# Optimization experiments

Measured on AMD Instinct MI355X. Metric: run time of the kernel, lower is better.

Reference implementation:

```python
import jax, jax.numpy as jnp
import numpy as np

N_NODES = 50000
N_EDGES = 800000
D_IN, D1, D2, D_OUT = 128, 150, 100, 64


def setup_inputs() -> dict:
    key = jax.random.key(0)
    ks = jax.random.split(key, 10)
    x = jax.random.normal(ks[0], (N_NODES, D_IN), dtype=jnp.float32)
    src = jax.random.randint(ks[1], (N_EDGES,), 0, N_NODES, dtype=jnp.int32)
    dst = jax.random.randint(ks[2], (N_EDGES,), 0, N_NODES, dtype=jnp.int32)
    s1 = 1.0 / np.sqrt(D_IN)
    s2 = 1.0 / np.sqrt(D1)
    s3 = 1.0 / np.sqrt(D2)
    W1 = jax.random.uniform(ks[3], (D_IN, D1), jnp.float32, -s1, s1)
    b1 = jnp.zeros((D1,), jnp.float32)
    Wn = jax.random.uniform(ks[4], (D1, D2), jnp.float32, -s2, s2)
    Ws = jax.random.uniform(ks[5], (D1, D2), jnp.float32, -s2, s2)
    b2 = jnp.zeros((D2,), jnp.float32)
    W3 = jax.random.uniform(ks[6], (D2, D_OUT), jnp.float32, -s3, s3)
    b3 = jnp.zeros((D_OUT,), jnp.float32)
    return {"x": x, "src": src, "dst": dst, "W1": W1, "b1": b1,
            "Wn": Wn, "Ws": Ws, "b2": b2, "W3": W3, "b3": b3}


def _degrees(src, dst, n):
    ones = jnp.ones(src.shape[0], jnp.float32)
    deg_out = jax.ops.segment_sum(ones, src, num_segments=n)
    deg_in = jax.ops.segment_sum(ones, dst, num_segments=n)
    return deg_out, deg_in


def reference(x, src, dst, W1, b1, Wn, Ws, b2, W3, b3):
    n = x.shape[0]
    deg_out, deg_in = _degrees(src, dst, n)
    norm_out = jax.lax.rsqrt(jnp.maximum(deg_out, 1.0))  # [N]
    norm_in = jax.lax.rsqrt(jnp.maximum(deg_in, 1.0))    # [N]

    # --- GraphConv (norm='both'): D_in^{-1/2} A D_out^{-1/2} X W + b ---
    h = x * norm_out[:, None]                                   # [N, D_IN]
    agg = jax.ops.segment_sum(h[src], dst, num_segments=n)      # [N, D_IN]
    h = (agg * norm_in[:, None]) @ W1 + b1                      # [N, D1]
    h = jax.nn.elu(h)

    # --- SAGEConv (mean): fc_self(h) + fc_neigh(mean_neighbors(h)) + b ---
    neigh_sum = jax.ops.segment_sum(h[src], dst, num_segments=n)  # [N, D1]
    neigh = neigh_sum / jnp.maximum(deg_in, 1.0)[:, None]
    h = h @ Ws + neigh @ Wn + b2                                  # [N, D2]
    h = jax.nn.elu(h)

    # --- Dense + ELU ---
    out = jax.nn.elu(h @ W3 + b3)                                 # [N, D_OUT]
    return out
```

## Files before the change

### kernel.cpp

```cpp
#include <hip/hip_runtime.h>
#include <math.h>

#define N_NODES 50000
#define N_EDGES 800000
#define D_IN 128
#define D1 150
#define LD1 152
#define D2 100
#define LDP 100
#define D_OUT 64
#define SLOT 64
#define HBLK 64
#define HBIN 12500

#define LDS_K 40

using short8 = __attribute__((ext_vector_type(8))) short;
using f32x4  = __attribute__((ext_vector_type(4))) float;

__device__ __forceinline__ float elu(float v) { return v > 0.0f ? v : expm1f(v); }

__device__ __forceinline__ void split_bf16(float a, unsigned short& h, unsigned short& l) {
    unsigned int bits = __float_as_uint(a);
    unsigned int hb = (bits + 0x8000u) >> 16;
    h = (unsigned short)hb;
    float r = a - __uint_as_float(hb << 16);
    l = (unsigned short)((__float_as_uint(r) + 0x8000u) >> 16);
}

__device__ __forceinline__ void split8(const float4 a, const float4 b, short8& h, short8& l) {
    float f[8] = {a.x, a.y, a.z, a.w, b.x, b.y, b.z, b.w};
#pragma unroll
    for (int i = 0; i < 8; ++i) {
        unsigned short hh, ll;
        split_bf16(f[i], hh, ll);
        h[i] = (short)hh; l[i] = (short)ll;
    }
}

__device__ __forceinline__ float4 g_load4(const float* p) { return *(const float4*)p; }

__device__ __forceinline__ float4 g_load4_guard(const float* row, int kbase, int Klim, bool rowok) {
    float4 v;
    v.x = (rowok && kbase + 0 < Klim) ? row[kbase + 0] : 0.0f;
    v.y = (rowok && kbase + 1 < Klim) ? row[kbase + 1] : 0.0f;
    v.z = (rowok && kbase + 2 < Klim) ? row[kbase + 2] : 0.0f;
    v.w = (rowok && kbase + 3 < Klim) ? row[kbase + 3] : 0.0f;
    return v;
}

__device__ __forceinline__ void barrier_lgkm() {
    asm volatile("s_waitcnt lgkmcnt(0)\n\ts_barrier" ::: "memory");
    __builtin_amdgcn_sched_barrier(0);
}

__global__ __launch_bounds__(256) void hist_kernel(const int* __restrict__ src,
                                                   unsigned int* __restrict__ partial) {
    __shared__ unsigned int bins[HBIN];
    int tid = threadIdx.x, b = blockIdx.x;
    for (int i = tid; i < HBIN; i += 256) bins[i] = 0u;
    __syncthreads();
    int e0 = b * (N_EDGES / HBLK);
    int e1 = e0 + (N_EDGES / HBLK);
    for (int e = e0 + tid; e < e1; e += 256) {
        int s = src[e];
        atomicAdd(&bins[s >> 2], 1u << ((s & 3) * 8));
    }
    __syncthreads();
    unsigned int* outp = partial + (size_t)b * HBIN;
    for (int i = tid; i < HBIN; i += 256) outp[i] = bins[i];
}

__global__ __launch_bounds__(256) void norm_kernel(const unsigned int* __restrict__ partial,
                                                   float* __restrict__ norm_out) {
    int i = blockIdx.x * blockDim.x + threadIdx.x;
    if (i >= HBIN) return;
    unsigned int acc = 0;
#pragma unroll
    for (int h = 0; h < HBLK; ++h) acc += partial[(size_t)h * HBIN + i];
#pragma unroll
    for (int j = 0; j < 4; ++j) {
        unsigned int dg = (acc >> (j * 8)) & 0xFF;
        norm_out[i * 4 + j] = rsqrtf(fmaxf((float)dg, 1.0f));
    }
}

__global__ void fill_kernel(const int* __restrict__ src, const int* __restrict__ dst,
                            int* __restrict__ cursor, unsigned short* __restrict__ slots) {
    int e = blockIdx.x * blockDim.x + threadIdx.x;
    if (e < N_EDGES) {
        int d = dst[e], s = src[e];
        int pos = atomicAdd(&cursor[d], 1);
        if (pos < SLOT) slots[d * SLOT + pos] = (unsigned short)s;
    }
}

__global__ __launch_bounds__(256) void gather_x(const float* __restrict__ x,
                                                const float* __restrict__ norm_out,
                                                const int* __restrict__ deg_in,
                                                const unsigned short* __restrict__ slots,
                                                float* __restrict__ agg) {
    int wave = threadIdx.x >> 6;
    int lane = threadIdx.x & 63;
    int half = lane >> 5;
    int c = lane & 31;
    int n = blockIdx.x * 4 + wave;
    if (n >= N_NODES) return;
    int beg = n * SLOT;
    int dg = deg_in[n]; if (dg > SLOT) dg = SLOT;
    int end = beg + dg;
    float4 acc = {0.0f, 0.0f, 0.0f, 0.0f};
    int e = beg + half;
    for (; e + 6 < end; e += 8) {
        int s0 = slots[e];
        int s1 = slots[e + 2];
        int s2 = slots[e + 4];
        int s3 = slots[e + 6];
        float w0 = norm_out[s0], w1 = norm_out[s1];
        float w2 = norm_out[s2], w3 = norm_out[s3];
        float4 v0 = ((const float4*)(x + (size_t)s0 * D_IN))[c];
        float4 v1 = ((const float4*)(x + (size_t)s1 * D_IN))[c];
        float4 v2 = ((const float4*)(x + (size_t)s2 * D_IN))[c];
        float4 v3 = ((const float4*)(x + (size_t)s3 * D_IN))[c];
        acc.x += v0.x * w0 + v1.x * w1 + v2.x * w2 + v3.x * w3;
        acc.y += v0.y * w0 + v1.y * w1 + v2.y * w2 + v3.y * w3;
        acc.z += v0.z * w0 + v1.z * w1 + v2.z * w2 + v3.z * w3;
        acc.w += v0.w * w0 + v1.w * w1 + v2.w * w2 + v3.w * w3;
    }
    for (; e < end; e += 2) {
        int s = slots[e];
        float w = norm_out[s];
        float4 v = ((const float4*)(x + (size_t)s * D_IN))[c];
        acc.x += v.x * w; acc.y += v.y * w; acc.z += v.z * w; acc.w += v.w * w;
    }
    acc.x += __shfl_xor(acc.x, 32);
    acc.y += __shfl_xor(acc.y, 32);
    acc.z += __shfl_xor(acc.z, 32);
    acc.w += __shfl_xor(acc.w, 32);
    if (half == 0) ((float4*)(agg + (size_t)n * D_IN))[c] = acc;
}

__global__ __launch_bounds__(256) void gather_p(const float* __restrict__ p,
                                                const int* __restrict__ deg_in,
                                                const unsigned short* __restrict__ slots,
                                                float* __restrict__ ns) {
    int wave = threadIdx.x >> 6;
    int lane = threadIdx.x & 63;
    int half = lane >> 5;
    int c = lane & 31;
    bool cv = c < D2 / 4;
    int n = blockIdx.x * 4 + wave;
    if (n >= N_NODES) return;
    int beg = n * SLOT;
    int dg = deg_in[n]; if (dg > SLOT) dg = SLOT;
    int end = beg + dg;
    float4 acc = {0.0f, 0.0f, 0.0f, 0.0f};
    if (cv) {
        int e = beg + half;
        for (; e + 6 < end; e += 8) {
            int s0 = slots[e];
            int s1 = slots[e + 2];
            int s2 = slots[e + 4];
            int s3 = slots[e + 6];
            float4 v0 = ((const float4*)(p + (size_t)s0 * LDP))[c];
            float4 v1 = ((const float4*)(p + (size_t)s1 * LDP))[c];
            float4 v2 = ((const float4*)(p + (size_t)s2 * LDP))[c];
            float4 v3 = ((const float4*)(p + (size_t)s3 * LDP))[c];
            acc.x += (v0.x + v1.x) + (v2.x + v3.x);
            acc.y += (v0.y + v1.y) + (v2.y + v3.y);
            acc.z += (v0.z + v1.z) + (v2.z + v3.z);
            acc.w += (v0.w + v1.w) + (v2.w + v3.w);
        }
        for (; e < end; e += 2) {
            int s = slots[e];
            float4 v = ((const float4*)(p + (size_t)s * LDP))[c];
            acc.x += v.x; acc.y += v.y; acc.z += v.z; acc.w += v.w;
        }
    }
    acc.x += __shfl_xor(acc.x, 32);
    acc.y += __shfl_xor(acc.y, 32);
    acc.z += __shfl_xor(acc.z, 32);
    acc.w += __shfl_xor(acc.w, 32);
    if (half == 0 && cv) ((float4*)(ns + (size_t)n * LDP))[c] = acc;
}


template <int K, int KP, int NW, int LDA, int PRE, int EPI, int LDC, int GROUP>
__global__ __launch_bounds__(256, 4)
void gemm_mfma(const float* __restrict__ A, const float* __restrict__ W,
               const float* __restrict__ nsrc, const int* __restrict__ deg,
               const float* __restrict__ bstage, const float* __restrict__ bepi,
               float* __restrict__ C) {
    constexpr int NSTEP = KP / 32;
    constexpr int MBLK = (N_NODES + 63) / 64;
    __shared__ __align__(16) unsigned short AsH[64][LDS_K];
    __shared__ __align__(16) unsigned short AsL[64][LDS_K];
    __shared__ __align__(16) unsigned short BsH[64][LDS_K];
    __shared__ __align__(16) unsigned short BsL[64][LDS_K];

    const int b = blockIdx.x;
    const int cxcd = b & 7;
    const int sIdx = b >> 3;
    const int jj = sIdx / GROUP;
    const int yy = sIdx - jj * GROUP;
    const int xb = cxcd + 8 * jj;
    if (xb >= MBLK) return;
    const int m0 = xb * 64;
    const int n0 = yy * 64;

    const int tid = threadIdx.x;
    const int arow = tid >> 2;
    const int ak = (tid & 3) * 8;
    const int grow = m0 + arow;
    const bool rowok = grow < N_NODES;
    const int bn = tid & 63;
    const int bkg = tid >> 6;
    const int bcol = n0 + bn;
    const int wid = tid >> 6;
    const int lane = tid & 63;
    const int wm = (wid >> 1) * 32;
    const int wn = (wid & 1) * 32;
    const int fr = lane & 15;
    const int fg = lane >> 4;

    float invd = 1.0f;
    if (PRE) {
        int dv = rowok ? deg[grow] : 1;
        invd = 1.0f / fmaxf((float)dv, 1.0f);
    }

    f32x4 acc[2][2];
#pragma unroll
    for (int i = 0; i < 2; ++i)
#pragma unroll
        for (int j = 0; j < 2; ++j) acc[i][j] = {0.0f, 0.0f, 0.0f, 0.0f};

    const float* arp = A + (size_t)grow * LDA;
    const float* nrp = PRE ? (nsrc + (size_t)grow * LDP) : nullptr;

    float4 pa[2][2], pn[2][2];
    float pb[2][8];

    {
        if (rowok && 32 <= K) {
            pa[0][0] = g_load4(arp + ak);
            pa[0][1] = g_load4(arp + ak + 4);
        } else {
            pa[0][0] = g_load4_guard(arp, ak, K, rowok);
            pa[0][1] = g_load4_guard(arp, ak + 4, K, rowok);
        }
        if (PRE) {
            if (rowok && 32 <= K) {
                pn[0][0] = g_load4(nrp + ak);
                pn[0][1] = g_load4(nrp + ak + 4);
            } else {
                pn[0][0] = g_load4_guard(nrp, ak, K, rowok);
                pn[0][1] = g_load4_guard(nrp, ak + 4, K, rowok);
            }
        }
#pragma unroll
        for (int kk = 0; kk < 8; ++kk) {
            int k = bkg * 8 + kk;
            pb[0][kk] = (k < K && bcol < NW) ? W[(size_t)k * NW + bcol] : 0.0f;
        }
    }

#pragma unroll
    for (int t = 0; t < NSTEP; ++t) {
        const int cur = t & 1, nxt = cur ^ 1;
        if (t + 1 < NSTEP) {
            const int k0n = (t + 1) * 32;
            if (rowok && k0n + 32 <= K) {
                pa[nxt][0] = g_load4(arp + k0n + ak);
                pa[nxt][1] = g_load4(arp + k0n + ak + 4);
            } else {
                pa[nxt][0] = g_load4_guard(arp, k0n + ak, K, rowok);
                pa[nxt][1] = g_load4_guard(arp, k0n + ak + 4, K, rowok);
            }
            if (PRE) {
                if (rowok && k0n + 32 <= K) {
                    pn[nxt][0] = g_load4(nrp + k0n + ak);
                    pn[nxt][1] = g_load4(nrp + k0n + ak + 4);
                } else {
                    pn[nxt][0] = g_load4_guard(nrp, k0n + ak, K, rowok);
                    pn[nxt][1] = g_load4_guard(nrp, k0n + ak + 4, K, rowok);
                }
            }
#pragma unroll
            for (int kk = 0; kk < 8; ++kk) {
                int k = k0n + bkg * 8 + kk;
                pb[nxt][kk] = (k < K && bcol < NW) ? W[(size_t)k * NW + bcol] : 0.0f;
            }
        }
        barrier_lgkm();
        {
            const int k0 = t * 32;
            float4 va0 = pa[cur][0], va1 = pa[cur][1];
            if (PRE) {
                const float4 vn0 = pn[cur][0], vn1 = pn[cur][1];
                if (k0 + 32 <= K) {
                    va0.x = elu(va0.x + bstage[k0 + ak + 0] + vn0.x * invd);
                    va0.y = elu(va0.y + bstage[k0 + ak + 1] + vn0.y * invd);
                    va0.z = elu(va0.z + bstage[k0 + ak + 2] + vn0.z * invd);
                    va0.w = elu(va0.w + bstage[k0 + ak + 3] + vn0.w * invd);
                    va1.x = elu(va1.x + bstage[k0 + ak + 4] + vn1.x * invd);
                    va1.y = elu(va1.y + bstage[k0 + ak + 5] + vn1.y * invd);
                    va1.z = elu(va1.z + bstage[k0 + ak + 6] + vn1.z * invd);
                    va1.w = elu(va1.w + bstage[k0 + ak + 7] + vn1.w * invd);
                } else {
                    va0.x = (k0 + ak + 0 < K) ? elu(va0.x + bstage[k0 + ak + 0] + vn0.x * invd) : 0.0f;
                    va0.y = (k0 + ak + 1 < K) ? elu(va0.y + bstage[k0 + ak + 1] + vn0.y * invd) : 0.0f;
                    va0.z = (k0 + ak + 2 < K) ? elu(va0.z + bstage[k0 + ak + 2] + vn0.z * invd) : 0.0f;
                    va0.w = (k0 + ak + 3 < K) ? elu(va0.w + bstage[k0 + ak + 3] + vn0.w * invd) : 0.0f;
                    va1.x = (k0 + ak + 4 < K) ? elu(va1.x + bstage[k0 + ak + 4] + vn1.x * invd) : 0.0f;
                    va1.y = (k0 + ak + 5 < K) ? elu(va1.y + bstage[k0 + ak + 5] + vn1.y * invd) : 0.0f;
                    va1.z = (k0 + ak + 6 < K) ? elu(va1.z + bstage[k0 + ak + 6] + vn1.z * invd) : 0.0f;
                    va1.w = (k0 + ak + 7 < K) ? elu(va1.w + bstage[k0 + ak + 7] + vn1.w * invd) : 0.0f;
                }
            }
            short8 h8, l8;
            split8(va0, va1, h8, l8);
            *(short8*)&AsH[arow][ak] = h8;
            *(short8*)&AsL[arow][ak] = l8;
            float4 vb0, vb1;
            vb0.x = pb[cur][0]; vb0.y = pb[cur][1]; vb0.z = pb[cur][2]; vb0.w = pb[cur][3];
            vb1.x = pb[cur][4]; vb1.y = pb[cur][5]; vb1.z = pb[cur][6]; vb1.w = pb[cur][7];
            split8(vb0, vb1, h8, l8);
            *(short8*)&BsH[bn][bkg * 8] = h8;
            *(short8*)&BsL[bn][bkg * 8] = l8;
        }
        barrier_lgkm();
        {
            short8 ah0 = *(const short8*)&AsH[wm + fr][fg * 8];
            short8 ah1 = *(const short8*)&AsH[wm + 16 + fr][fg * 8];
            short8 al0 = *(const short8*)&AsL[wm + fr][fg * 8];
            short8 al1 = *(const short8*)&AsL[wm + 16 + fr][fg * 8];
            short8 bh0 = *(const short8*)&BsH[wn + fr][fg * 8];
            short8 bh1 = *(const short8*)&BsH[wn + 16 + fr][fg * 8];
            short8 bl0 = *(const short8*)&BsL[wn + fr][fg * 8];
            short8 bl1 = *(const short8*)&BsL[wn + 16 + fr][fg * 8];
            acc[0][0] = __builtin_amdgcn_mfma_f32_16x16x32_bf16(ah0, bh0, acc[0][0], 0, 0, 0);
            acc[0][0] = __builtin_amdgcn_mfma_f32_16x16x32_bf16(al0, bh0, acc[0][0], 0, 0, 0);
            acc[0][0] = __builtin_amdgcn_mfma_f32_16x16x32_bf16(ah0, bl0, acc[0][0], 0, 0, 0);
            acc[0][1] = __builtin_amdgcn_mfma_f32_16x16x32_bf16(ah0, bh1, acc[0][1], 0, 0, 0);
            acc[0][1] = __builtin_amdgcn_mfma_f32_16x16x32_bf16(al0, bh1, acc[0][1], 0, 0, 0);
            acc[0][1] = __builtin_amdgcn_mfma_f32_16x16x32_bf16(ah0, bl1, acc[0][1], 0, 0, 0);
            acc[1][0] = __builtin_amdgcn_mfma_f32_16x16x32_bf16(ah1, bh0, acc[1][0], 0, 0, 0);
            acc[1][0] = __builtin_amdgcn_mfma_f32_16x16x32_bf16(al1, bh0, acc[1][0], 0, 0, 0);
            acc[1][0] = __builtin_amdgcn_mfma_f32_16x16x32_bf16(ah1, bl0, acc[1][0], 0, 0, 0);
            acc[1][1] = __builtin_amdgcn_mfma_f32_16x16x32_bf16(ah1, bh1, acc[1][1], 0, 0, 0);
            acc[1][1] = __builtin_amdgcn_mfma_f32_16x16x32_bf16(al1, bh1, acc[1][1], 0, 0, 0);
            acc[1][1] = __builtin_amdgcn_mfma_f32_16x16x32_bf16(ah1, bl1, acc[1][1], 0, 0, 0);
        }
    }

#pragma unroll
    for (int fi = 0; fi < 2; ++fi) {
#pragma unroll
        for (int r = 0; r < 4; ++r) {
            int row = m0 + wm + fi * 16 + fg * 4 + r;
            if (row >= N_NODES) continue;
            float rmul = 1.0f;
            if (EPI == 1) rmul = rsqrtf(fmaxf((float)deg[row], 1.0f));
#pragma unroll
            for (int fj = 0; fj < 2; ++fj) {
                int col = n0 + wn + fj * 16 + fr;
                if (col >= LDC) continue;
                float v = 0.0f;
                if (col < NW) {
                    v = acc[fi][fj][r];
                    if (EPI == 1) v = elu(v * rmul + bepi[col]);
                    else if (EPI == 3) v = elu(v + bepi[col]);
                }
                C[(size_t)row * LDC + col] = v;
            }
        }
    }
}

__global__ __launch_bounds__(256, 4)
void gemm_dual_mfma(const float* __restrict__ h1, const float* __restrict__ Wn,
                    const float* __restrict__ Ws, float* __restrict__ p,
                    float* __restrict__ h2pre) {
    constexpr int NSTEP = 5;
    constexpr int MBLK = (N_NODES + 63) / 64;
    __shared__ __align__(16) unsigned short AsH[64][LDS_K];
    __shared__ __align__(16) unsigned short AsL[64][LDS_K];
    __shared__ __align__(16) unsigned short BsH[64][LDS_K];
    __shared__ __align__(16) unsigned short BsL[64][LDS_K];

    const int b = blockIdx.x;
    const int cxcd = b & 7;
    const int sIdx = b >> 3;
    const int jj = sIdx >> 2;
    const int yy = sIdx & 3;
    const int xb = cxcd + 8 * jj;
    if (xb >= MBLK) return;
    const int m0 = xb * 64;
    const int n0 = (yy & 1) * 64;
    const float* W = (yy < 2) ? Wn : Ws;

    const int tid = threadIdx.x;
    const int arow = tid >> 2;
    const int ak = (tid & 3) * 8;
    const int grow = m0 + arow;
    const bool rowok = grow < N_NODES;
    const int bn = tid & 63;
    const int bkg = tid >> 6;
    const int bcol = n0 + bn;
    const int wid = tid >> 6;
    const int lane = tid & 63;
    const int wm = (wid >> 1) * 32;
    const int wn = (wid & 1) * 32;
    const int fr = lane & 15;
    const int fg = lane >> 4;

    f32x4 acc[2][2];
#pragma unroll
    for (int i = 0; i < 2; ++i)
#pragma unroll
        for (int j = 0; j < 2; ++j) acc[i][j] = {0.0f, 0.0f, 0.0f, 0.0f};

    const float* arp = h1 + (size_t)grow * LD1;

    float4 pa[2][2];
    float pb[2][8];

    {
        if (rowok) {
            pa[0][0] = g_load4(arp + ak);
            pa[0][1] = g_load4(arp + ak + 4);
        } else {
            pa[0][0] = g_load4_guard(arp, ak, D1, rowok);
            pa[0][1] = g_load4_guard(arp, ak + 4, D1, rowok);
        }
#pragma unroll
        for (int kk = 0; kk < 8; ++kk) {
            int k = bkg * 8 + kk;
            pb[0][kk] = (k < D1 && bcol < D2) ? W[(size_t)k * D2 + bcol] : 0.0f;
        }
    }

#pragma unroll
    for (int t = 0; t < NSTEP; ++t) {
        const int cur = t & 1, nxt = cur ^ 1;
        if (t + 1 < NSTEP) {
            const int k0n = (t + 1) * 32;
            if (rowok && k0n + 32 <= D1) {
                pa[nxt][0] = g_load4(arp + k0n + ak);
                pa[nxt][1] = g_load4(arp + k0n + ak + 4);
            } else {
                pa[nxt][0] = g_load4_guard(arp, k0n + ak, D1, rowok);
                pa[nxt][1] = g_load4_guard(arp, k0n + ak + 4, D1, rowok);
            }
#pragma unroll
            for (int kk = 0; kk < 8; ++kk) {
                int k = k0n + bkg * 8 + kk;
                pb[nxt][kk] = (k < D1 && bcol < D2) ? W[(size_t)k * D2 + bcol] : 0.0f;
            }
        }
        barrier_lgkm();
        {
            short8 h8, l8;
            split8(pa[cur][0], pa[cur][1], h8, l8);
            *(short8*)&AsH[arow][ak] = h8;
            *(short8*)&AsL[arow][ak] = l8;
            float4 vb0, vb1;
            vb0.x = pb[cur][0]; vb0.y = pb[cur][1]; vb0.z = pb[cur][2]; vb0.w = pb[cur][3];
            vb1.x = pb[cur][4]; vb1.y = pb[cur][5]; vb1.z = pb[cur][6]; vb1.w = pb[cur][7];
            split8(vb0, vb1, h8, l8);
            *(short8*)&BsH[bn][bkg * 8] = h8;
            *(short8*)&BsL[bn][bkg * 8] = l8;
        }
        barrier_lgkm();
        {
            short8 ah0 = *(const short8*)&AsH[wm + fr][fg * 8];
            short8 ah1 = *(const short8*)&AsH[wm + 16 + fr][fg * 8];
            short8 al0 = *(const short8*)&AsL[wm + fr][fg * 8];
            short8 al1 = *(const short8*)&AsL[wm + 16 + fr][fg * 8];
            short8 bh0 = *(const short8*)&BsH[wn + fr][fg * 8];
            short8 bh1 = *(const short8*)&BsH[wn + 16 + fr][fg * 8];
            short8 bl0 = *(const short8*)&BsL[wn + fr][fg * 8];
            short8 bl1 = *(const short8*)&BsL[wn + 16 + fr][fg * 8];
            acc[0][0] = __builtin_amdgcn_mfma_f32_16x16x32_bf16(ah0, bh0, acc[0][0], 0, 0, 0);
            acc[0][0] = __builtin_amdgcn_mfma_f32_16x16x32_bf16(al0, bh0, acc[0][0], 0, 0, 0);
            acc[0][0] = __builtin_amdgcn_mfma_f32_16x16x32_bf16(ah0, bl0, acc[0][0], 0, 0, 0);
            acc[0][1] = __builtin_amdgcn_mfma_f32_16x16x32_bf16(ah0, bh1, acc[0][1], 0, 0, 0);
            acc[0][1] = __builtin_amdgcn_mfma_f32_16x16x32_bf16(al0, bh1, acc[0][1], 0, 0, 0);
            acc[0][1] = __builtin_amdgcn_mfma_f32_16x16x32_bf16(ah0, bl1, acc[0][1], 0, 0, 0);
            acc[1][0] = __builtin_amdgcn_mfma_f32_16x16x32_bf16(ah1, bh0, acc[1][0], 0, 0, 0);
            acc[1][0] = __builtin_amdgcn_mfma_f32_16x16x32_bf16(al1, bh0, acc[1][0], 0, 0, 0);
            acc[1][0] = __builtin_amdgcn_mfma_f32_16x16x32_bf16(ah1, bl0, acc[1][0], 0, 0, 0);
            acc[1][1] = __builtin_amdgcn_mfma_f32_16x16x32_bf16(ah1, bh1, acc[1][1], 0, 0, 0);
            acc[1][1] = __builtin_amdgcn_mfma_f32_16x16x32_bf16(al1, bh1, acc[1][1], 0, 0, 0);
            acc[1][1] = __builtin_amdgcn_mfma_f32_16x16x32_bf16(ah1, bl1, acc[1][1], 0, 0, 0);
        }
    }

#pragma unroll
    for (int fi = 0; fi < 2; ++fi) {
#pragma unroll
        for (int r = 0; r < 4; ++r) {
            int row = m0 + wm + fi * 16 + fg * 4 + r;
            if (row >= N_NODES) continue;
#pragma unroll
            for (int fj = 0; fj < 2; ++fj) {
                int col = n0 + wn + fj * 16 + fr;
                float v = acc[fi][fj][r];
                if (col < D2) {
                    if (yy < 2) p[(size_t)row * LDP + col] = v;
                    else        h2pre[(size_t)row * D2 + col] = v;
                }
            }
        }
    }
}

extern "C" void kernel_launch(void* const* d_in, const int* in_sizes, int n_in,
                              void* d_out, int out_size, void* d_ws, size_t ws_size,
                              hipStream_t stream) {
    const float* x  = (const float*)d_in[0];
    const int* src  = (const int*)d_in[1];
    const int* dst  = (const int*)d_in[2];
    const float* W1 = (const float*)d_in[3];
    const float* b1 = (const float*)d_in[4];
    const float* Wn = (const float*)d_in[5];
    const float* Ws = (const float*)d_in[6];
    const float* b2 = (const float*)d_in[7];
    const float* W3 = (const float*)d_in[8];
    const float* b3 = (const float*)d_in[9];
    float* out = (float*)d_out;

    char* wsb = (char*)d_ws;
    unsigned int* partial = (unsigned int*)wsb;
    int*   cursor     = (int*)wsb + 800000;
    float* norm_out   = (float*)wsb + 850000;
    unsigned short* slots = (unsigned short*)((float*)wsb + 900000);
    float* agg        = (float*)wsb + 2500000;
    float* h1         = (float*)wsb + 8900000;
    float* h2pre      = (float*)wsb + 16500000;
    float* p          = agg;
    float* ns         = h1;
    int*   deg_in     = cursor;

    hipMemsetAsync(cursor, 0, N_NODES * sizeof(int), stream);

    hist_kernel<<<HBLK, 256, 0, stream>>>(src, partial);
    fill_kernel<<<(N_EDGES + 255) / 256, 256, 0, stream>>>(src, dst, cursor, slots);
    norm_kernel<<<(HBIN + 255) / 256, 256, 0, stream>>>(partial, norm_out);
    gather_x<<<(N_NODES + 3) / 4, 256, 0, stream>>>(x, norm_out, deg_in, slots, agg);

    const int MB = (N_NODES + 63) / 64;
    const int XG = (MB + 7) / 8;
    gemm_mfma<128, 128, 150, 128, 0, 1, LD1, 3><<<XG * 8 * 3, 256, 0, stream>>>(
        agg, W1, nullptr, deg_in, nullptr, b1, h1);
    gemm_dual_mfma<<<XG * 8 * 4, 256, 0, stream>>>(h1, Wn, Ws, p, h2pre);
    gather_p<<<(N_NODES + 3) / 4, 256, 0, stream>>>(p, deg_in, slots, ns);
    gemm_mfma<100, 128, 64, 100, 1, 3, D_OUT, 1><<<XG * 8, 256, 0, stream>>>(
        h2pre, W3, ns, deg_in, b2, b3, out);
}
```

Measured before the change: 330.4 us.

## Widen GEMM N-tiles so each block covers full output width

```diff
diff --git a/kernel.cpp b/kernel.cpp
--- a/kernel.cpp
+++ b/kernel.cpp
@@ -184,6 +184,265 @@
     if (half == 0 && cv) ((float4*)(ns + (size_t)n * LDP))[c] = acc;
 }
 
+__global__ __launch_bounds__(256, 4)
+void gemm1_mfma(const float* __restrict__ A, const float* __restrict__ W,
+                const int* __restrict__ deg, const float* __restrict__ bepi,
+                float* __restrict__ C) {
+    constexpr int MBLK = (N_NODES + 63) / 64;
+    __shared__ __align__(16) unsigned short AsH[64][LDS_K];
+    __shared__ __align__(16) unsigned short AsL[64][LDS_K];
+    __shared__ __align__(16) unsigned short BsH[160][LDS_K];
+    __shared__ __align__(16) unsigned short BsL[160][LDS_K];
+
+    const int b = blockIdx.x;
+    const int xb = (b & 7) + 8 * (b >> 3);
+    if (xb >= MBLK) return;
+    const int m0 = xb * 64;
+
+    const int tid = threadIdx.x;
+    const int arow = tid >> 2;
+    const int ak = (tid & 3) * 8;
+    const int grow = m0 + arow;
+    const bool rowok = grow < N_NODES;
+    const int kr2 = tid >> 4;
+    const int bc0 = (tid & 15) * 10;
+    const int wid = tid >> 6;
+    const int lane = tid & 63;
+    const int wm = (wid >> 1) * 32;
+    const int wn = (wid & 1) * 80;
+    const int fr = lane & 15;
+    const int fg = lane >> 4;
+
+    f32x4 acc[2][5];
+#pragma unroll
+    for (int i = 0; i < 2; ++i)
+#pragma unroll
+        for (int j = 0; j < 5; ++j) acc[i][j] = {0.0f, 0.0f, 0.0f, 0.0f};
+
+    const float* arp = A + (size_t)grow * D_IN;
+
+    float4 pa[2][2];
+    float pb[20];
+
+    {
+        float4 z = {0.0f, 0.0f, 0.0f, 0.0f};
+        pa[0][0] = rowok ? g_load4(arp + ak) : z;
+        pa[0][1] = rowok ? g_load4(arp + ak + 4) : z;
+        const int ka = 2 * kr2;
+#pragma unroll
+        for (int i = 0; i < 10; ++i) {
+            int cc = bc0 + i;
+            pb[i]      = (cc < D1) ? W[(size_t)ka * D1 + cc] : 0.0f;
+            pb[10 + i] = (cc < D1) ? W[(size_t)(ka + 1) * D1 + cc] : 0.0f;
+        }
+    }
+
+#pragma unroll
+    for (int t = 0; t < 4; ++t) {
+        const int cur = t & 1, nxt = cur ^ 1;
+        if (t < 3) {
+            const int k0n = (t + 1) * 32;
+            float4 z = {0.0f, 0.0f, 0.0f, 0.0f};
+            pa[nxt][0] = rowok ? g_load4(arp + k0n + ak) : z;
+            pa[nxt][1] = rowok ? g_load4(arp + k0n + ak + 4) : z;
+        }
+        barrier_lgkm();
+        {
+            short8 h8, l8;
+            split8(pa[cur][0], pa[cur][1], h8, l8);
+            *(short8*)&AsH[arow][ak] = h8;
+            *(short8*)&AsL[arow][ak] = l8;
+#pragma unroll
+            for (int i = 0; i < 10; ++i) {
+                int cc = bc0 + i;
+                unsigned short h0, l0, h1s, l1s;
+                split_bf16(pb[i], h0, l0);
+                split_bf16(pb[10 + i], h1s, l1s);
+                *(unsigned int*)&BsH[cc][2 * kr2] = (unsigned int)h0 | ((unsigned int)h1s << 16);
+                *(unsigned int*)&BsL[cc][2 * kr2] = (unsigned int)l0 | ((unsigned int)l1s << 16);
+            }
+            if (t < 3) {
+                const int ka = (t + 1) * 32 + 2 * kr2;
+#pragma unroll
+                for (int i = 0; i < 10; ++i) {
+                    int cc = bc0 + i;
+                    pb[i]      = (cc < D1) ? W[(size_t)ka * D1 + cc] : 0.0f;
+                    pb[10 + i] = (cc < D1) ? W[(size_t)(ka + 1) * D1 + cc] : 0.0f;
+                }
+            }
+        }
+        barrier_lgkm();
+        {
+            short8 ah0 = *(const short8*)&AsH[wm + fr][fg * 8];
+            short8 ah1 = *(const short8*)&AsH[wm + 16 + fr][fg * 8];
+            short8 al0 = *(const short8*)&AsL[wm + fr][fg * 8];
+            short8 al1 = *(const short8*)&AsL[wm + 16 + fr][fg * 8];
+#pragma unroll
+            for (int cf = 0; cf < 5; ++cf) {
+                short8 bh = *(const short8*)&BsH[wn + cf * 16 + fr][fg * 8];
+                short8 bl = *(const short8*)&BsL[wn + cf * 16 + fr][fg * 8];
+                acc[0][cf] = __builtin_amdgcn_mfma_f32_16x16x32_bf16(ah0, bh, acc[0][cf], 0, 0, 0);
+                acc[0][cf] = __builtin_amdgcn_mfma_f32_16x16x32_bf16(al0, bh, acc[0][cf], 0, 0, 0);
+                acc[0][cf] = __builtin_amdgcn_mfma_f32_16x16x32_bf16(ah0, bl, acc[0][cf], 0, 0, 0);
+                acc[1][cf] = __builtin_amdgcn_mfma_f32_16x16x32_bf16(ah1, bh, acc[1][cf], 0, 0, 0);
+                acc[1][cf] = __builtin_amdgcn_mfma_f32_16x16x32_bf16(al1, bh, acc[1][cf], 0, 0, 0);
+                acc[1][cf] = __builtin_amdgcn_mfma_f32_16x16x32_bf16(ah1, bl, acc[1][cf], 0, 0, 0);
+            }
+        }
+    }
+
+#pragma unroll
+    for (int fi = 0; fi < 2; ++fi) {
+#pragma unroll
+        for (int r = 0; r < 4; ++r) {
+            int row = m0 + wm + fi * 16 + fg * 4 + r;
+            if (row >= N_NODES) continue;
+            float rmul = rsqrtf(fmaxf((float)deg[row], 1.0f));
+#pragma unroll
+            for (int cf = 0; cf < 5; ++cf) {
+                int col = wn + cf * 16 + fr;
+                if (col >= LD1) continue;
+                float v = 0.0f;
+                if (col < D1) v = elu(acc[fi][cf][r] * rmul + bepi[col]);
+                C[(size_t)row * LD1 + col] = v;
+            }
+        }
+    }
+}
+
+__global__ __launch_bounds__(256, 4)
+void gemm_dual_mfma(const float* __restrict__ h1, const float* __restrict__ Wn,
+                    const float* __restrict__ Ws, float* __restrict__ p,
+                    float* __restrict__ h2pre) {
+    constexpr int MBLK = (N_NODES + 63) / 64;
+    __shared__ __align__(16) unsigned short AsH[64][LDS_K];
+    __shared__ __align__(16) unsigned short AsL[64][LDS_K];
+    __shared__ __align__(16) unsigned short BsH[128][LDS_K];
+    __shared__ __align__(16) unsigned short BsL[128][LDS_K];
+
+    const int b = blockIdx.x;
+    const int cx = b & 7;
+    const int sIdx = b >> 3;
+    const int jj = sIdx >> 1;
+    const int yy = sIdx & 1;
+    const int xb = cx + 8 * jj;
+    if (xb >= MBLK) return;
+    const int m0 = xb * 64;
+    const float* W = yy ? Ws : Wn;
+    float* Cc = yy ? h2pre : p;
+
+    const int tid = threadIdx.x;
+    const int arow = tid >> 2;
+    const int ak = (tid & 3) * 8;
+    const int grow = m0 + arow;
+    const bool rowok = grow < N_NODES;
+    const int bn = tid & 127;
+    const int khalf = (tid >> 7) * 16;
+    const bool bok = bn < D2;
+    const int wid = tid >> 6;
+    const int lane = tid & 63;
+    const int wm = (wid >> 1) * 32;
+    const int wn = (wid & 1) * 64;
+    const int fr = lane & 15;
+    const int fg = lane >> 4;
+
+    f32x4 acc[2][4];
+#pragma unroll
+    for (int i = 0; i < 2; ++i)
+#pragma unroll
+        for (int j = 0; j < 4; ++j) acc[i][j] = {0.0f, 0.0f, 0.0f, 0.0f};
+
+    const float* arp = h1 + (size_t)grow * LD1;
+
+    float4 pa[2][2];
+    float pb[16];
+
+    {
+        float4 z = {0.0f, 0.0f, 0.0f, 0.0f};
+        pa[0][0] = rowok ? g_load4(arp + ak) : z;
+        pa[0][1] = rowok ? g_load4(arp + ak + 4) : z;
+#pragma unroll
+        for (int kk = 0; kk < 16; ++kk) {
+            int k = khalf + kk;
+            pb[kk] = bok ? W[(size_t)k * D2 + bn] : 0.0f;
+        }
+    }
+
+#pragma unroll
+    for (int t = 0; t < 5; ++t) {
+        const int cur = t & 1, nxt = cur ^ 1;
+        if (t < 4) {
+            const int k0n = (t + 1) * 32;
+            if (rowok && k0n + 32 <= D1) {
+                pa[nxt][0] = g_load4(arp + k0n + ak);
+                pa[nxt][1] = g_load4(arp + k0n + ak + 4);
+            } else {
+                pa[nxt][0] = g_load4_guard(arp, k0n + ak, D1, rowok);
+                pa[nxt][1] = g_load4_guard(arp, k0n + ak + 4, D1, rowok);
+            }
+        }
+        barrier_lgkm();
+        {
+            short8 h8, l8;
+            split8(pa[cur][0], pa[cur][1], h8, l8);
+            *(short8*)&AsH[arow][ak] = h8;
+            *(short8*)&AsL[arow][ak] = l8;
+            short8 bh8a, bl8a, bh8b, bl8b;
+#pragma unroll
+            for (int kk = 0; kk < 8; ++kk) {
+                unsigned short hh, ll;
+                split_bf16(pb[kk], hh, ll);
+                bh8a[kk] = (short)hh; bl8a[kk] = (short)ll;
+                split_bf16(pb[8 + kk], hh, ll);
+                bh8b[kk] = (short)hh; bl8b[kk] = (short)ll;
+            }
+            *(short8*)&BsH[bn][khalf] = bh8a;
+            *(short8*)&BsH[bn][khalf + 8] = bh8b;
+            *(short8*)&BsL[bn][khalf] = bl8a;
+            *(short8*)&BsL[bn][khalf + 8] = bl8b;
+            if (t < 4) {
+                const int k0n = (t + 1) * 32;
+#pragma unroll
+                for (int kk = 0; kk < 16; ++kk) {
+                    int k = k0n + khalf + kk;
+                    pb[kk] = (bok && k < D1) ? W[(size_t)k * D2 + bn] : 0.0f;
+                }
+            }
+        }
+        barrier_lgkm();
+        {
+            short8 ah0 = *(const short8*)&AsH[wm + fr][fg * 8];
+            short8 ah1 = *(const short8*)&AsH[wm + 16 + fr][fg * 8];
+            short8 al0 = *(const short8*)&AsL[wm + fr][fg * 8];
+            short8 al1 = *(const short8*)&AsL[wm + 16 + fr][fg * 8];
+#pragma unroll
+            for (int fj = 0; fj < 4; ++fj) {
+                short8 bh = *(const short8*)&BsH[wn + fj * 16 + fr][fg * 8];
+                short8 bl = *(const short8*)&BsL[wn + fj * 16 + fr][fg * 8];
+                acc[0][fj] = __builtin_amdgcn_mfma_f32_16x16x32_bf16(ah0, bh, acc[0][fj], 0, 0, 0);
+                acc[0][fj] = __builtin_amdgcn_mfma_f32_16x16x32_bf16(al0, bh, acc[0][fj], 0, 0, 0);
+                acc[0][fj] = __builtin_amdgcn_mfma_f32_16x16x32_bf16(ah0, bl, acc[0][fj], 0, 0, 0);
+                acc[1][fj] = __builtin_amdgcn_mfma_f32_16x16x32_bf16(ah1, bh, acc[1][fj], 0, 0, 0);
+                acc[1][fj] = __builtin_amdgcn_mfma_f32_16x16x32_bf16(al1, bh, acc[1][fj], 0, 0, 0);
+                acc[1][fj] = __builtin_amdgcn_mfma_f32_16x16x32_bf16(ah1, bl, acc[1][fj], 0, 0, 0);
+            }
+        }
+    }
+
+#pragma unroll
+    for (int fi = 0; fi < 2; ++fi) {
+#pragma unroll
+        for (int r = 0; r < 4; ++r) {
+            int row = m0 + wm + fi * 16 + fg * 4 + r;
+            if (row >= N_NODES) continue;
+#pragma unroll
+            for (int fj = 0; fj < 4; ++fj) {
+                int col = wn + fj * 16 + fr;
+                if (col < D2) Cc[(size_t)row * D2 + col] = acc[fi][fj][r];
+            }
+        }
+    }
+}
 
 template <int K, int KP, int NW, int LDA, int PRE, int EPI, int LDC, int GROUP>
 __global__ __launch_bounds__(256, 4)
@@ -378,144 +637,6 @@
     }
 }
 
-__global__ __launch_bounds__(256, 4)
-void gemm_dual_mfma(const float* __restrict__ h1, const float* __restrict__ Wn,
-                    const float* __restrict__ Ws, float* __restrict__ p,
-                    float* __restrict__ h2pre) {
-    constexpr int NSTEP = 5;
-    constexpr int MBLK = (N_NODES + 63) / 64;
-    __shared__ __align__(16) unsigned short AsH[64][LDS_K];
-    __shared__ __align__(16) unsigned short AsL[64][LDS_K];
-    __shared__ __align__(16) unsigned short BsH[64][LDS_K];
-    __shared__ __align__(16) unsigned short BsL[64][LDS_K];
-
-    const int b = blockIdx.x;
-    const int cxcd = b & 7;
-    const int sIdx = b >> 3;
-    const int jj = sIdx >> 2;
-    const int yy = sIdx & 3;
-    const int xb = cxcd + 8 * jj;
-    if (xb >= MBLK) return;
-    const int m0 = xb * 64;
-    const int n0 = (yy & 1) * 64;
-    const float* W = (yy < 2) ? Wn : Ws;
-
-    const int tid = threadIdx.x;
-    const int arow = tid >> 2;
-    const int ak = (tid & 3) * 8;
-    const int grow = m0 + arow;
-    const bool rowok = grow < N_NODES;
-    const int bn = tid & 63;
-    const int bkg = tid >> 6;
-    const int bcol = n0 + bn;
-    const int wid = tid >> 6;
-    const int lane = tid & 63;
-    const int wm = (wid >> 1) * 32;
-    const int wn = (wid & 1) * 32;
-    const int fr = lane & 15;
-    const int fg = lane >> 4;
-
-    f32x4 acc[2][2];
-#pragma unroll
-    for (int i = 0; i < 2; ++i)
-#pragma unroll
-        for (int j = 0; j < 2; ++j) acc[i][j] = {0.0f, 0.0f, 0.0f, 0.0f};
-
-    const float* arp = h1 + (size_t)grow * LD1;
-
-    float4 pa[2][2];
-    float pb[2][8];
-
-    {
-        if (rowok) {
-            pa[0][0] = g_load4(arp + ak);
-            pa[0][1] = g_load4(arp + ak + 4);
-        } else {
-            pa[0][0] = g_load4_guard(arp, ak, D1, rowok);
-            pa[0][1] = g_load4_guard(arp, ak + 4, D1, rowok);
-        }
-#pragma unroll
-        for (int kk = 0; kk < 8; ++kk) {
-            int k = bkg * 8 + kk;
-            pb[0][kk] = (k < D1 && bcol < D2) ? W[(size_t)k * D2 + bcol] : 0.0f;
-        }
-    }
-
-#pragma unroll
-    for (int t = 0; t < NSTEP; ++t) {
-        const int cur = t & 1, nxt = cur ^ 1;
-        if (t + 1 < NSTEP) {
-            const int k0n = (t + 1) * 32;
-            if (rowok && k0n + 32 <= D1) {
-                pa[nxt][0] = g_load4(arp + k0n + ak);
-                pa[nxt][1] = g_load4(arp + k0n + ak + 4);
-            } else {
-                pa[nxt][0] = g_load4_guard(arp, k0n + ak, D1, rowok);
-                pa[nxt][1] = g_load4_guard(arp, k0n + ak + 4, D1, rowok);
-            }
-#pragma unroll
-            for (int kk = 0; kk < 8; ++kk) {
-                int k = k0n + bkg * 8 + kk;
-                pb[nxt][kk] = (k < D1 && bcol < D2) ? W[(size_t)k * D2 + bcol] : 0.0f;
-            }
-        }
-        barrier_lgkm();
-        {
-            short8 h8, l8;
-            split8(pa[cur][0], pa[cur][1], h8, l8);
-            *(short8*)&AsH[arow][ak] = h8;
-            *(short8*)&AsL[arow][ak] = l8;
-            float4 vb0, vb1;
-            vb0.x = pb[cur][0]; vb0.y = pb[cur][1]; vb0.z = pb[cur][2]; vb0.w = pb[cur][3];
-            vb1.x = pb[cur][4]; vb1.y = pb[cur][5]; vb1.z = pb[cur][6]; vb1.w = pb[cur][7];
-            split8(vb0, vb1, h8, l8);
-            *(short8*)&BsH[bn][bkg * 8] = h8;
-            *(short8*)&BsL[bn][bkg * 8] = l8;
-        }
-        barrier_lgkm();
-        {
-            short8 ah0 = *(const short8*)&AsH[wm + fr][fg * 8];
-            short8 ah1 = *(const short8*)&AsH[wm + 16 + fr][fg * 8];
-            short8 al0 = *(const short8*)&AsL[wm + fr][fg * 8];
-            short8 al1 = *(const short8*)&AsL[wm + 16 + fr][fg * 8];
-            short8 bh0 = *(const short8*)&BsH[wn + fr][fg * 8];
-            short8 bh1 = *(const short8*)&BsH[wn + 16 + fr][fg * 8];
-            short8 bl0 = *(const short8*)&BsL[wn + fr][fg * 8];
-            short8 bl1 = *(const short8*)&BsL[wn + 16 + fr][fg * 8];
-            acc[0][0] = __builtin_amdgcn_mfma_f32_16x16x32_bf16(ah0, bh0, acc[0][0], 0, 0, 0);
-            acc[0][0] = __builtin_amdgcn_mfma_f32_16x16x32_bf16(al0, bh0, acc[0][0], 0, 0, 0);
-            acc[0][0] = __builtin_amdgcn_mfma_f32_16x16x32_bf16(ah0, bl0, acc[0][0], 0, 0, 0);
-            acc[0][1] = __builtin_amdgcn_mfma_f32_16x16x32_bf16(ah0, bh1, acc[0][1], 0, 0, 0);
-            acc[0][1] = __builtin_amdgcn_mfma_f32_16x16x32_bf16(al0, bh1, acc[0][1], 0, 0, 0);
-            acc[0][1] = __builtin_amdgcn_mfma_f32_16x16x32_bf16(ah0, bl1, acc[0][1], 0, 0, 0);
-            acc[1][0] = __builtin_amdgcn_mfma_f32_16x16x32_bf16(ah1, bh0, acc[1][0], 0, 0, 0);
-            acc[1][0] = __builtin_amdgcn_mfma_f32_16x16x32_bf16(al1, bh0, acc[1][0], 0, 0, 0);
-            acc[1][0] = __builtin_amdgcn_mfma_f32_16x16x32_bf16(ah1, bl0, acc[1][0], 0, 0, 0);
-            acc[1][1] = __builtin_amdgcn_mfma_f32_16x16x32_bf16(ah1, bh1, acc[1][1], 0, 0, 0);
-            acc[1][1] = __builtin_amdgcn_mfma_f32_16x16x32_bf16(al1, bh1, acc[1][1], 0, 0, 0);
-            acc[1][1] = __builtin_amdgcn_mfma_f32_16x16x32_bf16(ah1, bl1, acc[1][1], 0, 0, 0);
-        }
-    }
-
-#pragma unroll
-    for (int fi = 0; fi < 2; ++fi) {
-#pragma unroll
-        for (int r = 0; r < 4; ++r) {
-            int row = m0 + wm + fi * 16 + fg * 4 + r;
-            if (row >= N_NODES) continue;
-#pragma unroll
-            for (int fj = 0; fj < 2; ++fj) {
-                int col = n0 + wn + fj * 16 + fr;
-                float v = acc[fi][fj][r];
-                if (col < D2) {
-                    if (yy < 2) p[(size_t)row * LDP + col] = v;
-                    else        h2pre[(size_t)row * D2 + col] = v;
-                }
-            }
-        }
-    }
-}
-
 extern "C" void kernel_launch(void* const* d_in, const int* in_sizes, int n_in,
                               void* d_out, int out_size, void* d_ws, size_t ws_size,
                               hipStream_t stream) {
@@ -552,9 +673,8 @@
 
     const int MB = (N_NODES + 63) / 64;
     const int XG = (MB + 7) / 8;
-    gemm_mfma<128, 128, 150, 128, 0, 1, LD1, 3><<<XG * 8 * 3, 256, 0, stream>>>(
-        agg, W1, nullptr, deg_in, nullptr, b1, h1);
-    gemm_dual_mfma<<<XG * 8 * 4, 256, 0, stream>>>(h1, Wn, Ws, p, h2pre);
+    gemm1_mfma<<<XG * 8, 256, 0, stream>>>(agg, W1, deg_in, b1, h1);
+    gemm_dual_mfma<<<XG * 8 * 2, 256, 0, stream>>>(h1, Wn, Ws, p, h2pre);
     gather_p<<<(N_NODES + 3) / 4, 256, 0, stream>>>(p, deg_in, slots, ns);
     gemm_mfma<100, 128, 64, 100, 1, 3, D_OUT, 1><<<XG * 8, 256, 0, stream>>>(
         h2pre, W3, ns, deg_in, b2, b3, out);
```

After: 346.0 us. +4.7%, slower.

## Fuse SAGE neighbor gather into final dense GEMM kernel

Applied to the files above, without the earlier changes.

```diff
diff --git a/kernel.cpp b/kernel.cpp
--- a/kernel.cpp
+++ b/kernel.cpp
@@ -140,51 +140,6 @@
     if (half == 0) ((float4*)(agg + (size_t)n * D_IN))[c] = acc;
 }
 
-__global__ __launch_bounds__(256) void gather_p(const float* __restrict__ p,
-                                                const int* __restrict__ deg_in,
-                                                const unsigned short* __restrict__ slots,
-                                                float* __restrict__ ns) {
-    int wave = threadIdx.x >> 6;
-    int lane = threadIdx.x & 63;
-    int half = lane >> 5;
-    int c = lane & 31;
-    bool cv = c < D2 / 4;
-    int n = blockIdx.x * 4 + wave;
-    if (n >= N_NODES) return;
-    int beg = n * SLOT;
-    int dg = deg_in[n]; if (dg > SLOT) dg = SLOT;
-    int end = beg + dg;
-    float4 acc = {0.0f, 0.0f, 0.0f, 0.0f};
-    if (cv) {
-        int e = beg + half;
-        for (; e + 6 < end; e += 8) {
-            int s0 = slots[e];
-            int s1 = slots[e + 2];
-            int s2 = slots[e + 4];
-            int s3 = slots[e + 6];
-            float4 v0 = ((const float4*)(p + (size_t)s0 * LDP))[c];
-            float4 v1 = ((const float4*)(p + (size_t)s1 * LDP))[c];
-            float4 v2 = ((const float4*)(p + (size_t)s2 * LDP))[c];
-            float4 v3 = ((const float4*)(p + (size_t)s3 * LDP))[c];
-            acc.x += (v0.x + v1.x) + (v2.x + v3.x);
-            acc.y += (v0.y + v1.y) + (v2.y + v3.y);
-            acc.z += (v0.z + v1.z) + (v2.z + v3.z);
-            acc.w += (v0.w + v1.w) + (v2.w + v3.w);
-        }
-        for (; e < end; e += 2) {
-            int s = slots[e];
-            float4 v = ((const float4*)(p + (size_t)s * LDP))[c];
-            acc.x += v.x; acc.y += v.y; acc.z += v.z; acc.w += v.w;
-        }
-    }
-    acc.x += __shfl_xor(acc.x, 32);
-    acc.y += __shfl_xor(acc.y, 32);
-    acc.z += __shfl_xor(acc.z, 32);
-    acc.w += __shfl_xor(acc.w, 32);
-    if (half == 0 && cv) ((float4*)(ns + (size_t)n * LDP))[c] = acc;
-}
-
-
 template <int K, int KP, int NW, int LDA, int PRE, int EPI, int LDC, int GROUP>
 __global__ __launch_bounds__(256, 4)
 void gemm_mfma(const float* __restrict__ A, const float* __restrict__ W,
@@ -516,6 +471,208 @@
     }
 }
 
+__global__ __launch_bounds__(256, 3)
+void gemm3_fused(const float* __restrict__ h2pre, const float* __restrict__ W3,
+                 const float* __restrict__ p, const int* __restrict__ deg,
+                 const unsigned short* __restrict__ slots,
+                 const float* __restrict__ b2, const float* __restrict__ b3,
+                 float* __restrict__ out) {
+    constexpr int K = 100, NSTEP = 4;
+    constexpr int MBLK = (N_NODES + 63) / 64;
+    __shared__ __align__(16) float Ns[64][100];
+    __shared__ __align__(16) unsigned short AsH[64][LDS_K];
+    __shared__ __align__(16) unsigned short AsL[64][LDS_K];
+    __shared__ __align__(16) unsigned short BsH[64][LDS_K];
+    __shared__ __align__(16) unsigned short BsL[64][LDS_K];
+
+    const int b = blockIdx.x;
+    const int xb = (b & 7) + 8 * (b >> 3);
+    if (xb >= MBLK) return;
+    const int m0 = xb * 64;
+
+    const int tid = threadIdx.x;
+    const int arow = tid >> 2;
+    const int ak = (tid & 3) * 8;
+    const int grow = m0 + arow;
+    const bool rowok = grow < N_NODES;
+    const int bn = tid & 63;
+    const int bkg = tid >> 6;
+    const int wid = tid >> 6;
+    const int lane = tid & 63;
+    const int wm = (wid >> 1) * 32;
+    const int wn = (wid & 1) * 32;
+    const int fr = lane & 15;
+    const int fg = lane >> 4;
+
+    f32x4 acc[2][2];
+#pragma unroll
+    for (int i = 0; i < 2; ++i)
+#pragma unroll
+        for (int j = 0; j < 2; ++j) acc[i][j] = {0.0f, 0.0f, 0.0f, 0.0f};
+
+    const float* arp = h2pre + (size_t)grow * D2;
+
+    float4 pa[2][2];
+    float pb[2][8];
+
+    {
+        if (rowok) {
+            pa[0][0] = g_load4(arp + ak);
+            pa[0][1] = g_load4(arp + ak + 4);
+        } else {
+            pa[0][0] = g_load4_guard(arp, ak, K, rowok);
+            pa[0][1] = g_load4_guard(arp, ak + 4, K, rowok);
+        }
+#pragma unroll
+        for (int kk = 0; kk < 8; ++kk) {
+            int k = bkg * 8 + kk;
+            pb[0][kk] = (k < K) ? W3[(size_t)k * D_OUT + bn] : 0.0f;
+        }
+    }
+
+    {
+        const int wave = tid >> 6;
+        const int half = lane >> 5;
+        const int c = lane & 31;
+        const bool cv = c < D2 / 4;
+        for (int rr = 0; rr < 16; ++rr) {
+            int n = m0 + wave * 16 + rr;
+            if (n >= N_NODES) break;
+            int beg = n * SLOT;
+            int dg = deg[n]; if (dg > SLOT) dg = SLOT;
+            int end = beg + dg;
+            float4 a4 = {0.0f, 0.0f, 0.0f, 0.0f};
+            if (cv) {
+                int e = beg + half;
+                for (; e + 6 < end; e += 8) {
+                    int s0 = slots[e];
+                    int s1 = slots[e + 2];
+                    int s2 = slots[e + 4];
+                    int s3 = slots[e + 6];
+                    float4 v0 = ((const float4*)(p + (size_t)s0 * LDP))[c];
+                    float4 v1 = ((const float4*)(p + (size_t)s1 * LDP))[c];
+                    float4 v2 = ((const float4*)(p + (size_t)s2 * LDP))[c];
+                    float4 v3 = ((const float4*)(p + (size_t)s3 * LDP))[c];
+                    a4.x += (v0.x + v1.x) + (v2.x + v3.x);
+                    a4.y += (v0.y + v1.y) + (v2.y + v3.y);
+                    a4.z += (v0.z + v1.z) + (v2.z + v3.z);
+                    a4.w += (v0.w + v1.w) + (v2.w + v3.w);
+                }
+                for (; e < end; e += 2) {
+                    int s = slots[e];
+                    float4 v = ((const float4*)(p + (size_t)s * LDP))[c];
+                    a4.x += v.x; a4.y += v.y; a4.z += v.z; a4.w += v.w;
+                }
+            }
+            a4.x += __shfl_xor(a4.x, 32);
+            a4.y += __shfl_xor(a4.y, 32);
+            a4.z += __shfl_xor(a4.z, 32);
+            a4.w += __shfl_xor(a4.w, 32);
+            if (half == 0 && cv) *(float4*)&Ns[wave * 16 + rr][c * 4] = a4;
+        }
+    }
+    barrier_lgkm();
+
+    float invd;
+    {
+        int dv = rowok ? deg[grow] : 1;
+        invd = 1.0f / fmaxf((float)dv, 1.0f);
+    }
+
+#pragma unroll
+    for (int t = 0; t < NSTEP; ++t) {
+        const int cur = t & 1, nxt = cur ^ 1;
+        if (t + 1 < NSTEP) {
+            const int k0n = (t + 1) * 32;
+            if (rowok && k0n + 32 <= K) {
+                pa[nxt][0] = g_load4(arp + k0n + ak);
+                pa[nxt][1] = g_load4(arp + k0n + ak + 4);
+            } else {
+                pa[nxt][0] = g_load4_guard(arp, k0n + ak, K, rowok);
+                pa[nxt][1] = g_load4_guard(arp, k0n + ak + 4, K, rowok);
+            }
+#pragma unroll
+            for (int kk = 0; kk < 8; ++kk) {
+                int k = k0n + bkg * 8 + kk;
+                pb[nxt][kk] = (k < K) ? W3[(size_t)k * D_OUT + bn] : 0.0f;
+            }
+        }
+        barrier_lgkm();
+        {
+            const int k0 = t * 32;
+            float4 va0 = pa[cur][0], va1 = pa[cur][1];
+            if (rowok && k0 + 32 <= K) {
+                const float4 n0 = *(const float4*)&Ns[arow][k0 + ak];
+                const float4 n1 = *(const float4*)&Ns[arow][k0 + ak + 4];
+                va0.x = elu(va0.x + b2[k0 + ak + 0] + n0.x * invd);
+                va0.y = elu(va0.y + b2[k0 + ak + 1] + n0.y * invd);
+                va0.z = elu(va0.z + b2[k0 + ak + 2] + n0.z * invd);
+                va0.w = elu(va0.w + b2[k0 + ak + 3] + n0.w * invd);
+                va1.x = elu(va1.x + b2[k0 + ak + 4] + n1.x * invd);
+                va1.y = elu(va1.y + b2[k0 + ak + 5] + n1.y * invd);
+                va1.z = elu(va1.z + b2[k0 + ak + 6] + n1.z * invd);
+                va1.w = elu(va1.w + b2[k0 + ak + 7] + n1.w * invd);
+            } else {
+                float av[8] = {va0.x, va0.y, va0.z, va0.w, va1.x, va1.y, va1.z, va1.w};
+#pragma unroll
+                for (int i = 0; i < 8; ++i) {
+                    int k = k0 + ak + i;
+                    av[i] = (rowok && k < K) ? elu(av[i] + b2[k] + Ns[arow][k] * invd) : 0.0f;
+                }
+                va0.x = av[0]; va0.y = av[1]; va0.z = av[2]; va0.w = av[3];
+                va1.x = av[4]; va1.y = av[5]; va1.z = av[6]; va1.w = av[7];
+            }
+            short8 h8, l8;
+            split8(va0, va1, h8, l8);
+            *(short8*)&AsH[arow][ak] = h8;
+            *(short8*)&AsL[arow][ak] = l8;
+            float4 vb0, vb1;
+            vb0.x = pb[cur][0]; vb0.y = pb[cur][1]; vb0.z = pb[cur][2]; vb0.w = pb[cur][3];
+            vb1.x = pb[cur][4]; vb1.y = pb[cur][5]; vb1.z = pb[cur][6]; vb1.w = pb[cur][7];
+            split8(vb0, vb1, h8, l8);
+            *(short8*)&BsH[bn][bkg * 8] = h8;
+            *(short8*)&BsL[bn][bkg * 8] = l8;
+        }
+        barrier_lgkm();
+        {
+            short8 ah0 = *(const short8*)&AsH[wm + fr][fg * 8];
+            short8 ah1 = *(const short8*)&AsH[wm + 16 + fr][fg * 8];
+            short8 al0 = *(const short8*)&AsL[wm + fr][fg * 8];
+            short8 al1 = *(const short8*)&AsL[wm + 16 + fr][fg * 8];
+            short8 bh0 = *(const short8*)&BsH[wn + fr][fg * 8];
+            short8 bh1 = *(const short8*)&BsH[wn + 16 + fr][fg * 8];
+            short8 bl0 = *(const short8*)&BsL[wn + fr][fg * 8];
+            short8 bl1 = *(const short8*)&BsL[wn + 16 + fr][fg * 8];
+            acc[0][0] = __builtin_amdgcn_mfma_f32_16x16x32_bf16(ah0, bh0, acc[0][0], 0, 0, 0);
+            acc[0][0] = __builtin_amdgcn_mfma_f32_16x16x32_bf16(al0, bh0, acc[0][0], 0, 0, 0);
+            acc[0][0] = __builtin_amdgcn_mfma_f32_16x16x32_bf16(ah0, bl0, acc[0][0], 0, 0, 0);
+            acc[0][1] = __builtin_amdgcn_mfma_f32_16x16x32_bf16(ah0, bh1, acc[0][1], 0, 0, 0);
+            acc[0][1] = __builtin_amdgcn_mfma_f32_16x16x32_bf16(al0, bh1, acc[0][1], 0, 0, 0);
+            acc[0][1] = __builtin_amdgcn_mfma_f32_16x16x32_bf16(ah0, bl1, acc[0][1], 0, 0, 0);
+            acc[1][0] = __builtin_amdgcn_mfma_f32_16x16x32_bf16(ah1, bh0, acc[1][0], 0, 0, 0);
+            acc[1][0] = __builtin_amdgcn_mfma_f32_16x16x32_bf16(al1, bh0, acc[1][0], 0, 0, 0);
+            acc[1][0] = __builtin_amdgcn_mfma_f32_16x16x32_bf16(ah1, bl0, acc[1][0], 0, 0, 0);
+            acc[1][1] = __builtin_amdgcn_mfma_f32_16x16x32_bf16(ah1, bh1, acc[1][1], 0, 0, 0);
+            acc[1][1] = __builtin_amdgcn_mfma_f32_16x16x32_bf16(al1, bh1, acc[1][1], 0, 0, 0);
+            acc[1][1] = __builtin_amdgcn_mfma_f32_16x16x32_bf16(ah1, bl1, acc[1][1], 0, 0, 0);
+        }
+    }
+
+#pragma unroll
+    for (int fi = 0; fi < 2; ++fi) {
+#pragma unroll
+        for (int r = 0; r < 4; ++r) {
+            int row = m0 + wm + fi * 16 + fg * 4 + r;
+            if (row >= N_NODES) continue;
+#pragma unroll
+            for (int fj = 0; fj < 2; ++fj) {
+                int col = wn + fj * 16 + fr;
+                out[(size_t)row * D_OUT + col] = elu(acc[fi][fj][r] + b3[col]);
+            }
+        }
+    }
+}
+
 extern "C" void kernel_launch(void* const* d_in, const int* in_sizes, int n_in,
                               void* d_out, int out_size, void* d_ws, size_t ws_size,
                               hipStream_t stream) {
@@ -540,7 +697,6 @@
     float* h1         = (float*)wsb + 8900000;
     float* h2pre      = (float*)wsb + 16500000;
     float* p          = agg;
-    float* ns         = h1;
     int*   deg_in     = cursor;
 
     hipMemsetAsync(cursor, 0, N_NODES * sizeof(int), stream);
@@ -555,7 +711,5 @@
     gemm_mfma<128, 128, 150, 128, 0, 1, LD1, 3><<<XG * 8 * 3, 256, 0, stream>>>(
         agg, W1, nullptr, deg_in, nullptr, b1, h1);
     gemm_dual_mfma<<<XG * 8 * 4, 256, 0, stream>>>(h1, Wn, Ws, p, h2pre);
-    gather_p<<<(N_NODES + 3) / 4, 256, 0, stream>>>(p, deg_in, slots, ns);
-    gemm_mfma<100, 128, 64, 100, 1, 3, D_OUT, 1><<<XG * 8, 256, 0, stream>>>(
-        h2pre, W3, ns, deg_in, b2, b3, out);
-}
+    gemm3_fused<<<XG * 8, 256, 0, stream>>>(h2pre, W3, p, deg_in, slots, b2, b3, out);
+}
```

After: 378.2 us. +14.4%, slower.

## Fold out-degree histogram into fill kernel via global atomics; raise GEMM occupancy

Applied to the files above, without the earlier changes.

```diff
diff --git a/kernel.cpp b/kernel.cpp
--- a/kernel.cpp
+++ b/kernel.cpp
@@ -10,8 +10,6 @@
 #define LDP 100
 #define D_OUT 64
 #define SLOT 64
-#define HBLK 64
-#define HBIN 12500
 
 #define LDS_K 40
 
@@ -54,45 +52,22 @@
     __builtin_amdgcn_sched_barrier(0);
 }
 
-__global__ __launch_bounds__(256) void hist_kernel(const int* __restrict__ src,
-                                                   unsigned int* __restrict__ partial) {
-    __shared__ unsigned int bins[HBIN];
-    int tid = threadIdx.x, b = blockIdx.x;
-    for (int i = tid; i < HBIN; i += 256) bins[i] = 0u;
-    __syncthreads();
-    int e0 = b * (N_EDGES / HBLK);
-    int e1 = e0 + (N_EDGES / HBLK);
-    for (int e = e0 + tid; e < e1; e += 256) {
-        int s = src[e];
-        atomicAdd(&bins[s >> 2], 1u << ((s & 3) * 8));
-    }
-    __syncthreads();
-    unsigned int* outp = partial + (size_t)b * HBIN;
-    for (int i = tid; i < HBIN; i += 256) outp[i] = bins[i];
-}
-
-__global__ __launch_bounds__(256) void norm_kernel(const unsigned int* __restrict__ partial,
-                                                   float* __restrict__ norm_out) {
-    int i = blockIdx.x * blockDim.x + threadIdx.x;
-    if (i >= HBIN) return;
-    unsigned int acc = 0;
-#pragma unroll
-    for (int h = 0; h < HBLK; ++h) acc += partial[(size_t)h * HBIN + i];
-#pragma unroll
-    for (int j = 0; j < 4; ++j) {
-        unsigned int dg = (acc >> (j * 8)) & 0xFF;
-        norm_out[i * 4 + j] = rsqrtf(fmaxf((float)dg, 1.0f));
-    }
-}
-
 __global__ void fill_kernel(const int* __restrict__ src, const int* __restrict__ dst,
-                            int* __restrict__ cursor, unsigned short* __restrict__ slots) {
+                            int* __restrict__ cursor, unsigned short* __restrict__ slots,
+                            unsigned int* __restrict__ deg_cnt) {
     int e = blockIdx.x * blockDim.x + threadIdx.x;
     if (e < N_EDGES) {
         int d = dst[e], s = src[e];
         int pos = atomicAdd(&cursor[d], 1);
         if (pos < SLOT) slots[d * SLOT + pos] = (unsigned short)s;
-    }
+        atomicAdd(&deg_cnt[s], 1u);
+    }
+}
+
+__global__ __launch_bounds__(256) void norm_kernel(const unsigned int* __restrict__ deg_cnt,
+                                                   float* __restrict__ norm_out) {
+    int i = blockIdx.x * blockDim.x + threadIdx.x;
+    if (i < N_NODES) norm_out[i] = rsqrtf(fmaxf((float)deg_cnt[i], 1.0f));
 }
 
 __global__ __launch_bounds__(256) void gather_x(const float* __restrict__ x,
@@ -184,9 +159,8 @@
     if (half == 0 && cv) ((float4*)(ns + (size_t)n * LDP))[c] = acc;
 }
 
-
 template <int K, int KP, int NW, int LDA, int PRE, int EPI, int LDC, int GROUP>
-__global__ __launch_bounds__(256, 4)
+__global__ __launch_bounds__(256, 6)
 void gemm_mfma(const float* __restrict__ A, const float* __restrict__ W,
                const float* __restrict__ nsrc, const int* __restrict__ deg,
                const float* __restrict__ bstage, const float* __restrict__ bepi,
@@ -378,7 +352,7 @@
     }
 }
 
-__global__ __launch_bounds__(256, 4)
+__global__ __launch_bounds__(256, 6)
 void gemm_dual_mfma(const float* __restrict__ h1, const float* __restrict__ Wn,
                     const float* __restrict__ Ws, float* __restrict__ p,
                     float* __restrict__ h2pre) {
@@ -532,7 +506,7 @@
     float* out = (float*)d_out;
 
     char* wsb = (char*)d_ws;
-    unsigned int* partial = (unsigned int*)wsb;
+    unsigned int* deg_cnt = (unsigned int*)wsb;
     int*   cursor     = (int*)wsb + 800000;
     float* norm_out   = (float*)wsb + 850000;
     unsigned short* slots = (unsigned short*)((float*)wsb + 900000);
@@ -544,10 +518,10 @@
     int*   deg_in     = cursor;
 
     hipMemsetAsync(cursor, 0, N_NODES * sizeof(int), stream);
-
-    hist_kernel<<<HBLK, 256, 0, stream>>>(src, partial);
-    fill_kernel<<<(N_EDGES + 255) / 256, 256, 0, stream>>>(src, dst, cursor, slots);
-    norm_kernel<<<(HBIN + 255) / 256, 256, 0, stream>>>(partial, norm_out);
+    hipMemsetAsync(deg_cnt, 0, N_NODES * sizeof(unsigned int), stream);
+
+    fill_kernel<<<(N_EDGES + 255) / 256, 256, 0, stream>>>(src, dst, cursor, slots, deg_cnt);
+    norm_kernel<<<(N_NODES + 255) / 256, 256, 0, stream>>>(deg_cnt, norm_out);
     gather_x<<<(N_NODES + 3) / 4, 256, 0, stream>>>(x, norm_out, deg_in, slots, agg);
 
     const int MB = (N_NODES + 63) / 64;
```

Measured after the change: 365.1 us. +10.5%, slower.
